# Kernel tuning notes

Hardware: AMD Instinct MI355X
Metric: run time of the kernel (lower is better)

Reference implementation:

```python
import jax, jax.numpy as jnp
import numpy as np

L, B, D, K = 12, 8192, 1024, 64


def setup_inputs() -> dict:
    key = jax.random.key(0)
    kx, kw = jax.random.split(key)
    x = jax.random.normal(kx, (L, B, D), dtype=jnp.float32)
    W = jax.random.normal(kw, (K, D), dtype=jnp.float32) * (1.0 / np.sqrt(D))
    b = jnp.zeros((K,), dtype=jnp.float32)
    return {"x": x, "W": W, "b": b}


def reference(x, W, b):
    # Original: for each bit i, Linear(D,1) applied per layer l, stacked,
    # mean over L, concat over bits -> [B, K], then tanh.
    # mean_l(x_l @ W_i + b_i) == mean_l(x)_b @ W_i + b_i, so fuse:
    xm = jnp.mean(x, axis=0)                      # [B, D]
    out = jnp.tanh(jnp.einsum('bd,kd->bk', xm, W) + b)  # [B, K]
    return out
```

## Files before the change

### kernel.cpp

```cpp
#include <hip/hip_runtime.h>
#include <hip/hip_bf16.h>
#include <cstdint>

#define NL 12
#define NB 8192
#define ND 1024
#define NK 64
#define TB 16

typedef __attribute__((ext_vector_type(8))) short bf16x8;
typedef __attribute__((ext_vector_type(4))) float f32x4;

__device__ __forceinline__ unsigned short f2bf(float f) {
  union { float f; unsigned int u; } v; v.f = f;
  unsigned int u = v.u;
  u += 0x7FFFu + ((u >> 16) & 1u);
  return (unsigned short)(u >> 16);
}

__global__ void __launch_bounds__(256)
fused_mean_gemm_tanh(const float* __restrict__ x, const float* __restrict__ W,
                     const float* __restrict__ bias, float* __restrict__ out) {
  __shared__ __align__(16) unsigned char xs[TB * 2048];

  const int tid = threadIdx.x;
  const int b0 = blockIdx.x * TB;

  const float4* x4 = (const float4*)x;
  for (int i = 0; i < TB; ++i) {
    const float4* p = x4 + (size_t)(b0 + i) * (ND / 4) + tid;
    float4 a = p[0];
#pragma unroll
    for (int l = 1; l < NL; ++l) {
      float4 v = p[(size_t)l * (NB * (ND / 4))];
      a.x += v.x; a.y += v.y; a.z += v.z; a.w += v.w;
    }
    unsigned int lo = (unsigned)f2bf(a.x) | ((unsigned)f2bf(a.y) << 16);
    unsigned int hi = (unsigned)f2bf(a.z) | ((unsigned)f2bf(a.w) << 16);
    int byte = i * 2048 + tid * 8;
    byte ^= (i & 7) << 4;
    uint2 u; u.x = lo; u.y = hi;
    *(uint2*)(xs + byte) = u;
  }
  __syncthreads();

  const int lane = tid & 63;
  const int w    = tid >> 6;
  const int mn   = lane & 15;
  const int g    = lane >> 4;
  const int kn0  = w * 16;

  f32x4 acc = {0.f, 0.f, 0.f, 0.f};
  const float* Wrow = W + (size_t)(kn0 + mn) * ND;
  const int abase = mn * 2048 + 16 * g;
  const int axor  = (mn & 7) << 4;

#pragma unroll 4
  for (int step = 0; step < 32; ++step) {
    int byte = (abase + 64 * step) ^ axor;
    bf16x8 afrag = *(const bf16x8*)(xs + byte);

    const float* wp = Wrow + 32 * step + 8 * g;
    float4 w0 = *(const float4*)(wp);
    float4 w1 = *(const float4*)(wp + 4);
    bf16x8 bfrag;
    bfrag[0] = (short)f2bf(w0.x); bfrag[1] = (short)f2bf(w0.y);
    bfrag[2] = (short)f2bf(w0.z); bfrag[3] = (short)f2bf(w0.w);
    bfrag[4] = (short)f2bf(w1.x); bfrag[5] = (short)f2bf(w1.y);
    bfrag[6] = (short)f2bf(w1.z); bfrag[7] = (short)f2bf(w1.w);

    acc = __builtin_amdgcn_mfma_f32_16x16x32_bf16(afrag, bfrag, acc, 0, 0, 0);
  }

  const float bv = bias[kn0 + mn];
#pragma unroll
  for (int r = 0; r < 4; ++r) {
    int row = 4 * g + r;
    float val = tanhf(acc[r] * (1.0f / 12.0f) + bv);
    out[(size_t)(b0 + row) * NK + kn0 + mn] = val;
  }
}

extern "C" void kernel_launch(void* const* d_in, const int* in_sizes, int n_in,
                              void* d_out, int out_size, void* d_ws, size_t ws_size,
                              hipStream_t stream) {
  const float* x    = (const float*)d_in[0];
  const float* W    = (const float*)d_in[1];
  const float* bias = (const float*)d_in[2];
  float* out = (float*)d_out;

  dim3 grid(NB / TB);
  dim3 block(256);
  hipLaunchKernelGGL(fused_mean_gemm_tanh, grid, block, 0, stream,
                     x, W, bias, out);
}
```

Measured before the change: 85.38 us.

## Pre-convert W to bf16, double threads per block, split-K across waves

A separate kernel converts W to bf16 once into workspace, so the GEMM loop no longer repeats the fp32 load and bf16 conversion in every block. The main kernel uses 512 threads: each half sums a different set of rows of x over layers, using nontemporal loads. Eight waves split the K reduction in half, and the partial accumulators are combined through shared memory. This adds a second launch and an extra barrier, in exchange for more memory-level parallelism on the bandwidth-bound mean over layers.

```diff
diff --git a/kernel.cpp b/kernel.cpp
--- a/kernel.cpp
+++ b/kernel.cpp
@@ -19,65 +19,82 @@
 }
 
 __global__ void __launch_bounds__(256)
-fused_mean_gemm_tanh(const float* __restrict__ x, const float* __restrict__ W,
+wconv_kernel(const float* __restrict__ W, uint2* __restrict__ Wb) {
+  int i = blockIdx.x * 256 + threadIdx.x;
+  f32x4 v = *((const f32x4*)W + i);
+  uint2 u;
+  u.x = (unsigned)f2bf(v[0]) | ((unsigned)f2bf(v[1]) << 16);
+  u.y = (unsigned)f2bf(v[2]) | ((unsigned)f2bf(v[3]) << 16);
+  Wb[i] = u;
+}
+
+__global__ void __launch_bounds__(512, 4)
+fused_mean_gemm_tanh(const float* __restrict__ x,
+                     const unsigned short* __restrict__ Wb,
                      const float* __restrict__ bias, float* __restrict__ out) {
   __shared__ __align__(16) unsigned char xs[TB * 2048];
+  __shared__ f32x4 pred[4 * 64];
 
   const int tid = threadIdx.x;
   const int b0 = blockIdx.x * TB;
 
-  const float4* x4 = (const float4*)x;
-  for (int i = 0; i < TB; ++i) {
-    const float4* p = x4 + (size_t)(b0 + i) * (ND / 4) + tid;
-    float4 a = p[0];
+  const int rhalf = tid >> 8;
+  const int t     = tid & 255;
+  const f32x4* x4 = (const f32x4*)x;
+
+  for (int s = 0; s < 8; ++s) {
+    const int i = 2 * s + rhalf;
+    const f32x4* p = x4 + (size_t)(b0 + i) * (ND / 4) + t;
+    f32x4 a = __builtin_nontemporal_load(p);
 #pragma unroll
     for (int l = 1; l < NL; ++l) {
-      float4 v = p[(size_t)l * (NB * (ND / 4))];
-      a.x += v.x; a.y += v.y; a.z += v.z; a.w += v.w;
+      f32x4 v = __builtin_nontemporal_load(p + (size_t)l * (NB * (ND / 4)));
+      a += v;
     }
-    unsigned int lo = (unsigned)f2bf(a.x) | ((unsigned)f2bf(a.y) << 16);
-    unsigned int hi = (unsigned)f2bf(a.z) | ((unsigned)f2bf(a.w) << 16);
-    int byte = i * 2048 + tid * 8;
+    unsigned int lo = (unsigned)f2bf(a[0]) | ((unsigned)f2bf(a[1]) << 16);
+    unsigned int hi = (unsigned)f2bf(a[2]) | ((unsigned)f2bf(a[3]) << 16);
+    int byte = i * 2048 + t * 8;
     byte ^= (i & 7) << 4;
     uint2 u; u.x = lo; u.y = hi;
     *(uint2*)(xs + byte) = u;
   }
   __syncthreads();
 
-  const int lane = tid & 63;
-  const int w    = tid >> 6;
-  const int mn   = lane & 15;
-  const int g    = lane >> 4;
-  const int kn0  = w * 16;
+  const int lane  = tid & 63;
+  const int w     = tid >> 6;
+  const int ktile = w & 3;
+  const int khalf = w >> 2;
+  const int mn    = lane & 15;
+  const int g     = lane >> 4;
+  const int kn0   = ktile * 16;
 
   f32x4 acc = {0.f, 0.f, 0.f, 0.f};
-  const float* Wrow = W + (size_t)(kn0 + mn) * ND;
+  const unsigned short* Wrow = Wb + (size_t)(kn0 + mn) * ND;
   const int abase = mn * 2048 + 16 * g;
   const int axor  = (mn & 7) << 4;
 
 #pragma unroll 4
-  for (int step = 0; step < 32; ++step) {
+  for (int ss = 0; ss < 16; ++ss) {
+    const int step = khalf * 16 + ss;
     int byte = (abase + 64 * step) ^ axor;
     bf16x8 afrag = *(const bf16x8*)(xs + byte);
-
-    const float* wp = Wrow + 32 * step + 8 * g;
-    float4 w0 = *(const float4*)(wp);
-    float4 w1 = *(const float4*)(wp + 4);
-    bf16x8 bfrag;
-    bfrag[0] = (short)f2bf(w0.x); bfrag[1] = (short)f2bf(w0.y);
-    bfrag[2] = (short)f2bf(w0.z); bfrag[3] = (short)f2bf(w0.w);
-    bfrag[4] = (short)f2bf(w1.x); bfrag[5] = (short)f2bf(w1.y);
-    bfrag[6] = (short)f2bf(w1.z); bfrag[7] = (short)f2bf(w1.w);
-
+    bf16x8 bfrag = *(const bf16x8*)(Wrow + 32 * step + 8 * g);
     acc = __builtin_amdgcn_mfma_f32_16x16x32_bf16(afrag, bfrag, acc, 0, 0, 0);
   }
 
-  const float bv = bias[kn0 + mn];
+  if (w >= 4) pred[(w - 4) * 64 + lane] = acc;
+  __syncthreads();
+
+  if (w < 4) {
+    f32x4 o = pred[w * 64 + lane];
+    acc += o;
+    const float bv = bias[kn0 + mn];
 #pragma unroll
-  for (int r = 0; r < 4; ++r) {
-    int row = 4 * g + r;
-    float val = tanhf(acc[r] * (1.0f / 12.0f) + bv);
-    out[(size_t)(b0 + row) * NK + kn0 + mn] = val;
+    for (int r = 0; r < 4; ++r) {
+      int row = 4 * g + r;
+      float val = tanhf(acc[r] * (1.0f / 12.0f) + bv);
+      out[(size_t)(b0 + row) * NK + kn0 + mn] = val;
+    }
   }
 }
 
@@ -88,9 +105,10 @@
   const float* W    = (const float*)d_in[1];
   const float* bias = (const float*)d_in[2];
   float* out = (float*)d_out;
+  unsigned short* Wb = (unsigned short*)d_ws;
 
-  dim3 grid(NB / TB);
-  dim3 block(256);
-  hipLaunchKernelGGL(fused_mean_gemm_tanh, grid, block, 0, stream,
-                     x, W, bias, out);
+  hipLaunchKernelGGL(wconv_kernel, dim3(NK * ND / 4 / 256), dim3(256), 0,
+                     stream, W, (uint2*)Wb);
+  hipLaunchKernelGGL(fused_mean_gemm_tanh, dim3(NB / TB), dim3(512), 0, stream,
+                     x, Wb, bias, out);
 }
```

Result: faster. 74.05 us (-13.3%).
